# Kernel optimization log

Measured on AMD Instinct MI355X. Metric: run time of the kernel, lower is better.

The kernel has to match this reference:

```python
import jax, jax.numpy as jnp
import numpy as np

IH, IW, HEADS, DIM_HEAD = 32, 32, 8, 48
N = IH * IW
SCALE = DIM_HEAD ** -0.5
EPS = 1e-5


def _relative_index():
    # static precompute of relative distance indices, shape [N, N] int32
    yy, xx = np.meshgrid(np.arange(IH), np.arange(IW), indexing='ij')
    coords = np.stack([yy.ravel(), xx.ravel()])  # [2, N]
    rel = coords[:, :, None] - coords[:, None, :]  # [2, N, N]
    dist = np.ceil(np.sqrt(rel[0] ** 2 + rel[1] ** 2)).astype(np.int32)
    return jnp.asarray(dist)

REL_INDEX = _relative_index()


def _layernorm(x, w, b):
    mu = jnp.mean(x, axis=-1, keepdims=True)
    var = jnp.var(x, axis=-1, keepdims=True)
    return (x - mu) * jax.lax.rsqrt(var + EPS) * w + b


def setup_inputs() -> dict:
    key = jax.random.key(0)
    ks = jax.random.split(key, 8)
    d, inner, hid = 384, HEADS * DIM_HEAD, 1536
    return {
        'x': jax.random.normal(ks[0], (16, IH, IW, d), jnp.float32),
        'ln1_w': jnp.ones((d,), jnp.float32),
        'ln1_b': jnp.zeros((d,), jnp.float32),
        'w_qkv': jax.random.normal(ks[1], (d, 3 * inner), jnp.float32) * (d ** -0.5),
        'bias_table': jax.random.normal(ks[2], (45, HEADS), jnp.float32) * 0.02,
        'w_out': jax.random.normal(ks[3], (inner, d), jnp.float32) * (inner ** -0.5),
        'b_out': jnp.zeros((d,), jnp.float32),
        'ln2_w': jnp.ones((d,), jnp.float32),
        'ln2_b': jnp.zeros((d,), jnp.float32),
        'w1': jax.random.normal(ks[4], (d, hid), jnp.float32) * (d ** -0.5),
        'b1': jnp.zeros((hid,), jnp.float32),
        'w2': jax.random.normal(ks[5], (hid, d), jnp.float32) * (hid ** -0.5),
        'b2': jnp.zeros((d,), jnp.float32),
    }


def reference(x, ln1_w, ln1_b, w_qkv, bias_table, w_out, b_out,
              ln2_w, ln2_b, w1, b1, w2, b2):
    b = x.shape[0]
    xt = x.reshape(b, N, -1)  # b (ih iw) c

    # --- attention branch (PreNorm) ---
    h = _layernorm(xt, ln1_w, ln1_b)
    qkv = h @ w_qkv  # [b, N, 3*inner]
    q, k, v = jnp.split(qkv, 3, axis=-1)
    q = q.reshape(b, N, HEADS, DIM_HEAD).transpose(0, 2, 1, 3)
    k = k.reshape(b, N, HEADS, DIM_HEAD).transpose(0, 2, 1, 3)
    v = v.reshape(b, N, HEADS, DIM_HEAD).transpose(0, 2, 1, 3)
    dots = jnp.einsum('bhnd,bhmd->bhnm', q, k) * SCALE
    rel_bias = bias_table[REL_INDEX]  # [N, N, heads] gather
    dots = dots + rel_bias.transpose(2, 0, 1)[None]  # [1, h, N, N]
    attn = jax.nn.softmax(dots, axis=-1)
    out = jnp.einsum('bhnm,bhmd->bhnd', attn, v)
    out = out.transpose(0, 2, 1, 3).reshape(b, N, HEADS * DIM_HEAD)
    out = out @ w_out + b_out
    xt = xt + out

    # --- FFN branch (PreNorm) ---
    h = _layernorm(xt, ln2_w, ln2_b)
    h = jax.nn.gelu(h @ w1 + b1, approximate=False) @ w2 + b2
    xt = xt + h
    return xt.reshape(x.shape)
```

## Files before the change

### kernel.cpp

```cpp
#include <hip/hip_runtime.h>
#include <hip/hip_bf16.h>
#include <math.h>

typedef __bf16 bf16;
typedef __bf16 bf16x8 __attribute__((ext_vector_type(8)));
typedef __bf16 bf16x4 __attribute__((ext_vector_type(4)));
typedef float  f32x4  __attribute__((ext_vector_type(4)));

#define D_MODEL 384
#define HID     1536
#define NSEQ    1024
#define ROWS    16384
#define HEADS   8
#define DH      48
#define SCALE   0.14433756729740643f
#define MFIX    8.0f
#define BTAB_N  3969
#define BTAB_P  3972
#define KVT     4608
#define QP_BH   (NSEQ * DH)
#define KP_BH   (16 * KVT)

__device__ __forceinline__ void gload16(const void* g, void* l) {
    __builtin_amdgcn_global_load_lds((const __attribute__((address_space(1))) void*)g,
                                     (__attribute__((address_space(3))) void*)l, 16, 0, 0);
}

__device__ __forceinline__ float fast_gelu(float x) {
    float u = 0.7978845608f * fmaf(0.044715f * x * x, x, x);
    float e = __expf(2.f * u);
    float t = 1.f - 2.f * __builtin_amdgcn_rcpf(e + 1.f);
    return 0.5f * x * (1.f + t);
}

__global__ __launch_bounds__(256)
void bias_prep_kernel(const float* __restrict__ bias_table, float* __restrict__ Btab)
{
    int idx = blockIdx.x * 256 + threadIdx.x;
    if (idx >= BTAB_N) return;
    int dy = idx / 63 - 31, dx = idx % 63 - 31;
    int s2 = dy * dy + dx * dx;
    int r = (int)ceilf(sqrtf((float)s2));
    while (r * r < s2) ++r;
    while (r > 0 && (r - 1) * (r - 1) >= s2) --r;
#pragma unroll
    for (int h = 0; h < HEADS; ++h)
        Btab[h * BTAB_P + idx] = bias_table[r * HEADS + h] - MFIX;
}

__global__ __launch_bounds__(256)
void pack_init_kernel(bf16* __restrict__ Kp, bf16* __restrict__ Vp)
{
    const int bid = blockIdx.x, tid = threadIdx.x;
    if (bid < 512) {
        int row = bid * 256 + tid;
        bf16x8 z = {};
        bf16* p = Kp + (size_t)row * 72 + 48;
        *(bf16x8*)(p) = z;  *(bf16x8*)(p + 8) = z;  *(bf16x8*)(p + 16) = z;
    } else {
        int idx = (bid - 512) * 256 + tid;
        int tile = idx >> 4, rr = idx & 15;
        bf16 o = (bf16)1.f;
        bf16x8 ones = {o, o, o, o, o, o, o, o};
        bf16* p = Vp + (size_t)tile * KVT + (48 + rr) * 72;
#pragma unroll
        for (int c = 0; c < 9; ++c) *(bf16x8*)(p + c * 8) = ones;
    }
}

__global__ __launch_bounds__(256)
void wtrans_kernel(const float* __restrict__ in, bf16* __restrict__ out, int K, int N)
{
    __shared__ float T[64][65];
    const int k0 = blockIdx.y * 64, n0 = blockIdx.x * 64;
    const int rr = threadIdx.x >> 4, rc = threadIdx.x & 15;
#pragma unroll
    for (int i = 0; i < 4; ++i) {
        float4 v = *(const float4*)(in + (size_t)(k0 + rr + i * 16) * N + n0 + rc * 4);
        T[rr + i * 16][rc * 4 + 0] = v.x;  T[rr + i * 16][rc * 4 + 1] = v.y;
        T[rr + i * 16][rc * 4 + 2] = v.z;  T[rr + i * 16][rc * 4 + 3] = v.w;
    }
    __syncthreads();
#pragma unroll
    for (int i = 0; i < 4; ++i) {
        int n = rr + i * 16, kc = rc * 4;
        bf16x4 o;
        o[0] = (bf16)T[kc + 0][n];  o[1] = (bf16)T[kc + 1][n];
        o[2] = (bf16)T[kc + 2][n];  o[3] = (bf16)T[kc + 3][n];
        *(bf16x4*)(out + (size_t)(n0 + n) * K + k0 + kc) = o;
    }
}

__global__ __launch_bounds__(64)
void ln_kernel(const float* __restrict__ x, const float* __restrict__ w,
               const float* __restrict__ b, bf16* __restrict__ out)
{
    int row  = blockIdx.x;
    int lane = threadIdx.x;
    const float* xr = x + (size_t)row * D_MODEL;

    float v[6], s = 0.f, ss = 0.f;
#pragma unroll
    for (int i = 0; i < 6; ++i) {
        v[i] = xr[lane + i * 64];
        s  += v[i];
        ss += v[i] * v[i];
    }
#pragma unroll
    for (int off = 32; off; off >>= 1) {
        s  += __shfl_xor(s,  off);
        ss += __shfl_xor(ss, off);
    }
    float mu   = s * (1.f / D_MODEL);
    float var  = ss * (1.f / D_MODEL) - mu * mu;
    float rstd = rsqrtf(var + 1e-5f);

    bf16* orow = out + (size_t)row * D_MODEL;
#pragma unroll
    for (int i = 0; i < 6; ++i) {
        int c = lane + i * 64;
        orow[c] = (bf16)((v[i] - mu) * rstd * w[c] + b[c]);
    }
}

template<int EPI, typename CT>
__global__ __launch_bounds__(256)
void gemm3_kernel(const bf16* __restrict__ A, const bf16* __restrict__ BT,
                  CT* __restrict__ C, const float* __restrict__ bias,
                  const float* __restrict__ res, int nxblk, int Nn, int K,
                  bf16* __restrict__ qp, bf16* __restrict__ kp, bf16* __restrict__ vp)
{
    __shared__ alignas(16) bf16 As[128][64];
    __shared__ alignas(16) bf16 Bs[128][64];

    const int bid  = blockIdx.x;
    const int xcd  = bid & 7;
    const int slot = bid >> 3;
    const int yy   = slot / nxblk;
    const int m0   = (yy * 8 + xcd) * 128;
    const int n0   = (slot - yy * nxblk) * 128;

    const int tid  = threadIdx.x;
    const int w    = tid >> 6;
    const int lane = tid & 63;
    const int quad = lane >> 4;
    const int l16  = lane & 15;

    const int srow = lane >> 3;
    const int scol = (lane & 7) * 8;

    f32x4 acc[4][4] = {};

    for (int kt = 0; kt < K; kt += 64) {
        __syncthreads();
#pragma unroll
        for (int c = 0; c < 4; ++c) {
            const int ch = w * 4 + c;
            gload16(A  + (size_t)(m0 + ch * 8 + srow) * K + kt + scol, &As[ch * 8][0]);
            gload16(BT + (size_t)(n0 + ch * 8 + srow) * K + kt + scol, &Bs[ch * 8][0]);
        }
        __syncthreads();

#pragma unroll
        for (int kk = 0; kk < 2; ++kk) {
            bf16x8 af[4], bfr[4];
#pragma unroll
            for (int mt = 0; mt < 4; ++mt)
                af[mt] = *(const bf16x8*)(&As[(w & 1) * 64 + mt * 16 + l16][kk * 32 + quad * 8]);
#pragma unroll
            for (int nt = 0; nt < 4; ++nt)
                bfr[nt] = *(const bf16x8*)(&Bs[(w >> 1) * 64 + nt * 16 + l16][kk * 32 + quad * 8]);
#pragma unroll
            for (int mt = 0; mt < 4; ++mt)
#pragma unroll
                for (int nt = 0; nt < 4; ++nt)
                    acc[mt][nt] = __builtin_amdgcn_mfma_f32_16x16x32_bf16(
                        af[mt], bfr[nt], acc[mt][nt], 0, 0, 0);
        }
    }

#pragma unroll
    for (int mt = 0; mt < 4; ++mt) {
#pragma unroll
        for (int nt = 0; nt < 4; ++nt) {
            const int c0 = n0 + (w >> 1) * 64 + nt * 16;
            const int c  = c0 + l16;
            float bi = (EPI == 1 || EPI == 2) ? bias[c] : 0.f;
#pragma unroll
            for (int r = 0; r < 4; ++r) {
                int row = m0 + (w & 1) * 64 + mt * 16 + quad * 4 + r;
                float v = acc[mt][nt][r] + bi;
                if (EPI == 1) {
                    v += res[(size_t)row * Nn + c];
                    C[(size_t)row * Nn + c] = (CT)v;
                } else if (EPI == 2) {
                    v = fast_gelu(v);
                    C[(size_t)row * Nn + c] = (CT)v;
                } else {
                    int b   = row >> 10, seq = row & 1023;
                    if (c0 < 384) {
                        int h = c / 48, d = c - h * 48;
                        qp[(size_t)(b * 8 + h) * QP_BH + seq * 48 + d] = (bf16)(v * SCALE);
                    } else if (c0 < 768) {
                        int ck = c - 384;
                        int h = ck / 48, d = ck - h * 48;
                        kp[(size_t)(b * 8 + h) * KP_BH + (seq >> 6) * KVT
                           + (seq & 63) * 72 + d] = (bf16)v;
                    } else {
                        int cv = c - 768;
                        int h = cv / 48, d = cv - h * 48;
                        vp[(size_t)(b * 8 + h) * KP_BH + (seq >> 6) * KVT
                           + d * 72 + (seq & 63)] = (bf16)v;
                    }
                }
            }
        }
    }
}

__global__ __launch_bounds__(256)
void attn_kernel(const bf16* __restrict__ Qp, const bf16* __restrict__ Kp,
                 const bf16* __restrict__ Vp, const float* __restrict__ Btab,
                 bf16* __restrict__ out)
{
    __shared__ alignas(16) bf16 Ks[64][72];
    __shared__ alignas(16) bf16 Vs[64][72];
    __shared__ alignas(16) bf16 Ps[4][2][16][72];
    __shared__ alignas(16) float B2f[BTAB_P];

    const int bid  = blockIdx.x;
    const int xcd  = bid & 7;
    const int slot = bid >> 3;
    const int qc   = slot & 7;
    const int bh   = (slot >> 3) * 8 + xcd;
    const int q0   = qc * 128;
    const int tid  = threadIdx.x;
    const int wave = tid >> 6;
    const int lane = tid & 63;
    const int quad = lane >> 4;
    const int l16  = lane & 15;
    const int b    = bh >> 3, h = bh & 7;

    {
        const char* src = (const char*)(Btab + h * BTAB_P);
#pragma unroll
        for (int it = 0; it < 4; ++it) {
            int off = it * 4096 + tid * 16;
            if (off < BTAB_P * 4)
                gload16(src + off, (char*)B2f + it * 4096 + wave * 1024);
        }
    }

    bf16x8 qf0[2], qf1[2];
    int pi[2];
#pragma unroll
    for (int s = 0; s < 2; ++s) {
        int qrow = q0 + s * 64 + wave * 16 + l16;
        const bf16* qptr = Qp + (size_t)bh * QP_BH + qrow * 48;
        qf0[s] = *(const bf16x8*)(qptr + quad * 8);
#pragma unroll
        for (int c = 0; c < 8; ++c) qf1[s][c] = (bf16)0.f;
        if (quad < 2) qf1[s] = *(const bf16x8*)(qptr + 32 + quad * 8);
        pi[s] = (qrow >> 5) * 63 + (qrow & 31) + 31 * 63 + 31;
    }

    f32x4 o_acc[2][4] = {};

    for (int t = 0; t < 16; ++t) {
        const int n0 = t * 64;
        const bf16* kbase = Kp + (size_t)(bh * 16 + t) * KVT;
        const bf16* vbase = Vp + (size_t)(bh * 16 + t) * KVT;
        __syncthreads();
        for (int i = wave; i < 9; i += 4) {
            gload16(kbase + i * 512 + lane * 8, (bf16*)Ks + i * 512);
            gload16(vbase + i * 512 + lane * 8, (bf16*)Vs + i * 512);
        }
        __syncthreads();

        f32x4 sa[2][4] = {};
#pragma unroll
        for (int nt = 0; nt < 4; ++nt) {
            bf16x8 a0 = *(const bf16x8*)(&Ks[nt * 16 + l16][quad * 8]);
            bf16x8 a1 = *(const bf16x8*)(&Ks[nt * 16 + l16][32 + quad * 8]);
#pragma unroll
            for (int s = 0; s < 2; ++s) {
                sa[s][nt] = __builtin_amdgcn_mfma_f32_16x16x32_bf16(a0, qf0[s], sa[s][nt], 0, 0, 0);
                sa[s][nt] = __builtin_amdgcn_mfma_f32_16x16x32_bf16(a1, qf1[s], sa[s][nt], 0, 0, 0);
            }
        }

#pragma unroll
        for (int s = 0; s < 2; ++s)
#pragma unroll
            for (int nt = 0; nt < 4; ++nt) {
                const int j0 = n0 + nt * 16 + quad * 4;
                const int ib = pi[s] - ((j0 >> 5) * 63 + (j0 & 31));
                bf16x4 pk;
#pragma unroll
                for (int r = 0; r < 4; ++r)
                    pk[r] = (bf16)__expf(sa[s][nt][r] + B2f[ib - r]);
                *(bf16x4*)(&Ps[wave][s][l16][nt * 16 + quad * 4]) = pk;
            }

#pragma unroll
        for (int kk = 0; kk < 2; ++kk) {
            bf16x8 vf[4];
#pragma unroll
            for (int d = 0; d < 4; ++d)
                vf[d] = *(const bf16x8*)(&Vs[d * 16 + l16][kk * 32 + quad * 8]);
#pragma unroll
            for (int s = 0; s < 2; ++s) {
                bf16x8 pf = *(const bf16x8*)(&Ps[wave][s][l16][kk * 32 + quad * 8]);
#pragma unroll
                for (int d = 0; d < 4; ++d)
                    o_acc[s][d] = __builtin_amdgcn_mfma_f32_16x16x32_bf16(
                        pf, vf[d], o_acc[s][d], 0, 0, 0);
            }
        }
    }

#pragma unroll
    for (int s = 0; s < 2; ++s)
#pragma unroll
        for (int r = 0; r < 4; ++r) {
            float inv = 1.f / o_acc[s][3][r];
            int row = q0 + s * 64 + wave * 16 + quad * 4 + r;
            bf16* orow = out + ((size_t)b * NSEQ + row) * D_MODEL + h * DH;
#pragma unroll
            for (int d = 0; d < 3; ++d)
                orow[d * 16 + l16] = (bf16)(o_acc[s][d][r] * inv);
        }
}

extern "C" void kernel_launch(void* const* d_in, const int* in_sizes, int n_in,
                              void* d_out, int out_size, void* d_ws, size_t ws_size,
                              hipStream_t stream)
{
    const float* x          = (const float*)d_in[0];
    const float* ln1_w      = (const float*)d_in[1];
    const float* ln1_b      = (const float*)d_in[2];
    const float* w_qkv      = (const float*)d_in[3];
    const float* bias_table = (const float*)d_in[4];
    const float* w_out      = (const float*)d_in[5];
    const float* b_out      = (const float*)d_in[6];
    const float* ln2_w      = (const float*)d_in[7];
    const float* ln2_b      = (const float*)d_in[8];
    const float* w1         = (const float*)d_in[9];
    const float* b1         = (const float*)d_in[10];
    const float* w2         = (const float*)d_in[11];
    const float* b2         = (const float*)d_in[12];
    float* out = (float*)d_out;

    bf16* regA  = (bf16*)d_ws;
    bf16* Qpack = regA;
    bf16* Kpack = regA + 6291456;
    bf16* Vpack = regA + 15728640;
    bf16* regB  = regA + (size_t)ROWS * HID;
    bf16* wqkvT = regB + (size_t)ROWS * D_MODEL;
    bf16* woutT = wqkvT + 1152 * 384;
    bf16* w1T   = woutT + 384 * 384;
    bf16* w2T   = w1T + 1536 * 384;
    float* Btab = (float*)(w2T + 384 * 1536);
    float* x1   = out;

    bias_prep_kernel<<<(BTAB_N + 255) / 256, 256, 0, stream>>>(bias_table, Btab);
    pack_init_kernel<<<640, 256, 0, stream>>>(Kpack, Vpack);
    wtrans_kernel<<<dim3(1152 / 64, 384 / 64), 256, 0, stream>>>(w_qkv, wqkvT, 384, 1152);
    wtrans_kernel<<<dim3(384 / 64, 384 / 64), 256, 0, stream>>>(w_out, woutT, 384, 384);
    wtrans_kernel<<<dim3(1536 / 64, 384 / 64), 256, 0, stream>>>(w1, w1T, 384, 1536);
    wtrans_kernel<<<dim3(384 / 64, 1536 / 64), 256, 0, stream>>>(w2, w2T, 1536, 384);

    ln_kernel<<<ROWS, 64, 0, stream>>>(x, ln1_w, ln1_b, regB);
    gemm3_kernel<3, bf16><<<(1152 / 128) * (ROWS / 128), 256, 0, stream>>>(
        regB, wqkvT, (bf16*)nullptr, nullptr, nullptr, 1152 / 128, 1152, D_MODEL,
        Qpack, Kpack, Vpack);
    attn_kernel<<<1024, 256, 0, stream>>>(Qpack, Kpack, Vpack, Btab, regB);
    gemm3_kernel<1, float><<<(D_MODEL / 128) * (ROWS / 128), 256, 0, stream>>>(
        regB, woutT, x1, b_out, x, D_MODEL / 128, D_MODEL, D_MODEL,
        nullptr, nullptr, nullptr);
    ln_kernel<<<ROWS, 64, 0, stream>>>(x1, ln2_w, ln2_b, regB);
    gemm3_kernel<2, bf16><<<(HID / 128) * (ROWS / 128), 256, 0, stream>>>(
        regB, w1T, regA, b1, nullptr, HID / 128, HID, D_MODEL,
        nullptr, nullptr, nullptr);
    gemm3_kernel<1, float><<<(D_MODEL / 128) * (ROWS / 128), 256, 0, stream>>>(
        regA, w2T, out, b2, x1, D_MODEL / 128, D_MODEL, HID,
        nullptr, nullptr, nullptr);
}
```

Baseline: 329.9 us.

## Shrink attention LDS with bf16 bias table, exp2 softmax, and wave priority

Stores the relative-position bias table as bf16 pre-scaled by log2(e) and folds log2(e) into the Q scale. The softmax then uses a native exp2 instead of expf, and the constant shift moves into the score accumulator initialisation. The P staging buffer is halved by processing the two query sub-tiles one after another, and MFMA sections are wrapped in s_setprio. Launch bounds now request 4 blocks per CU. Together these cut LDS use and per-element ALU work to raise occupancy, at some cost in bias precision.

```diff
diff --git a/kernel.cpp b/kernel.cpp
--- a/kernel.cpp
+++ b/kernel.cpp
@@ -14,9 +14,11 @@
 #define HEADS   8
 #define DH      48
 #define SCALE   0.14433756729740643f
-#define MFIX    8.0f
+#define LOG2E   1.4426950408889634f
+#define QSCALE  (SCALE * LOG2E)
+#define M0      (-8.0f * LOG2E)
 #define BTAB_N  3969
-#define BTAB_P  3972
+#define BTAB_P  4096
 #define KVT     4608
 #define QP_BH   (NSEQ * DH)
 #define KP_BH   (16 * KVT)
@@ -34,7 +36,7 @@
 }
 
 __global__ __launch_bounds__(256)
-void bias_prep_kernel(const float* __restrict__ bias_table, float* __restrict__ Btab)
+void bias_prep_kernel(const float* __restrict__ bias_table, bf16* __restrict__ Btab)
 {
     int idx = blockIdx.x * 256 + threadIdx.x;
     if (idx >= BTAB_N) return;
@@ -45,7 +47,7 @@
     while (r > 0 && (r - 1) * (r - 1) >= s2) --r;
 #pragma unroll
     for (int h = 0; h < HEADS; ++h)
-        Btab[h * BTAB_P + idx] = bias_table[r * HEADS + h] - MFIX;
+        Btab[h * BTAB_P + idx] = (bf16)(bias_table[r * HEADS + h] * LOG2E);
 }
 
 __global__ __launch_bounds__(256)
@@ -200,7 +202,7 @@
                     int b   = row >> 10, seq = row & 1023;
                     if (c0 < 384) {
                         int h = c / 48, d = c - h * 48;
-                        qp[(size_t)(b * 8 + h) * QP_BH + seq * 48 + d] = (bf16)(v * SCALE);
+                        qp[(size_t)(b * 8 + h) * QP_BH + seq * 48 + d] = (bf16)(v * QSCALE);
                     } else if (c0 < 768) {
                         int ck = c - 384;
                         int h = ck / 48, d = ck - h * 48;
@@ -218,15 +220,15 @@
     }
 }
 
-__global__ __launch_bounds__(256)
+__global__ __launch_bounds__(256, 4)
 void attn_kernel(const bf16* __restrict__ Qp, const bf16* __restrict__ Kp,
-                 const bf16* __restrict__ Vp, const float* __restrict__ Btab,
+                 const bf16* __restrict__ Vp, const bf16* __restrict__ Btab,
                  bf16* __restrict__ out)
 {
     __shared__ alignas(16) bf16 Ks[64][72];
     __shared__ alignas(16) bf16 Vs[64][72];
-    __shared__ alignas(16) bf16 Ps[4][2][16][72];
-    __shared__ alignas(16) float B2f[BTAB_P];
+    __shared__ alignas(16) bf16 Ps[4][16][72];
+    __shared__ alignas(16) bf16 B2h[BTAB_P];
 
     const int bid  = blockIdx.x;
     const int xcd  = bid & 7;
@@ -242,13 +244,9 @@
     const int b    = bh >> 3, h = bh & 7;
 
     {
-        const char* src = (const char*)(Btab + h * BTAB_P);
-#pragma unroll
-        for (int it = 0; it < 4; ++it) {
-            int off = it * 4096 + tid * 16;
-            if (off < BTAB_P * 4)
-                gload16(src + off, (char*)B2f + it * 4096 + wave * 1024);
-        }
+        const char* src = (const char*)(Btab + (size_t)h * BTAB_P);
+        gload16(src + tid * 16,        (char*)B2h + wave * 1024);
+        gload16(src + 4096 + tid * 16, (char*)B2h + 4096 + wave * 1024);
     }
 
     bf16x8 qf0[2], qf1[2];
@@ -277,7 +275,14 @@
         }
         __syncthreads();
 
-        f32x4 sa[2][4] = {};
+        f32x4 sa[2][4];
+#pragma unroll
+        for (int s = 0; s < 2; ++s)
+#pragma unroll
+            for (int nt = 0; nt < 4; ++nt)
+                sa[s][nt] = (f32x4){M0, M0, M0, M0};
+
+        __builtin_amdgcn_s_setprio(1);
 #pragma unroll
         for (int nt = 0; nt < 4; ++nt) {
             bf16x8 a0 = *(const bf16x8*)(&Ks[nt * 16 + l16][quad * 8]);
@@ -288,9 +293,10 @@
                 sa[s][nt] = __builtin_amdgcn_mfma_f32_16x16x32_bf16(a1, qf1[s], sa[s][nt], 0, 0, 0);
             }
         }
-
-#pragma unroll
-        for (int s = 0; s < 2; ++s)
+        __builtin_amdgcn_s_setprio(0);
+
+#pragma unroll
+        for (int s = 0; s < 2; ++s) {
 #pragma unroll
             for (int nt = 0; nt < 4; ++nt) {
                 const int j0 = n0 + nt * 16 + quad * 4;
@@ -298,24 +304,24 @@
                 bf16x4 pk;
 #pragma unroll
                 for (int r = 0; r < 4; ++r)
-                    pk[r] = (bf16)__expf(sa[s][nt][r] + B2f[ib - r]);
-                *(bf16x4*)(&Ps[wave][s][l16][nt * 16 + quad * 4]) = pk;
+                    pk[r] = (bf16)__builtin_amdgcn_exp2f(sa[s][nt][r] + (float)B2h[ib - r]);
+                *(bf16x4*)(&Ps[wave][l16][nt * 16 + quad * 4]) = pk;
             }
 
-#pragma unroll
-        for (int kk = 0; kk < 2; ++kk) {
-            bf16x8 vf[4];
-#pragma unroll
-            for (int d = 0; d < 4; ++d)
-                vf[d] = *(const bf16x8*)(&Vs[d * 16 + l16][kk * 32 + quad * 8]);
-#pragma unroll
-            for (int s = 0; s < 2; ++s) {
-                bf16x8 pf = *(const bf16x8*)(&Ps[wave][s][l16][kk * 32 + quad * 8]);
+            __builtin_amdgcn_s_setprio(1);
+#pragma unroll
+            for (int kk = 0; kk < 2; ++kk) {
+                bf16x8 vf[4];
+#pragma unroll
+                for (int d = 0; d < 4; ++d)
+                    vf[d] = *(const bf16x8*)(&Vs[d * 16 + l16][kk * 32 + quad * 8]);
+                bf16x8 pf = *(const bf16x8*)(&Ps[wave][l16][kk * 32 + quad * 8]);
 #pragma unroll
                 for (int d = 0; d < 4; ++d)
                     o_acc[s][d] = __builtin_amdgcn_mfma_f32_16x16x32_bf16(
                         pf, vf[d], o_acc[s][d], 0, 0, 0);
             }
+            __builtin_amdgcn_s_setprio(0);
         }
     }
 
@@ -360,7 +366,7 @@
     bf16* woutT = wqkvT + 1152 * 384;
     bf16* w1T   = woutT + 384 * 384;
     bf16* w2T   = w1T + 1536 * 384;
-    float* Btab = (float*)(w2T + 384 * 1536);
+    bf16* Btab  = w2T + 384 * 1536;
     float* x1   = out;
 
     bias_prep_kernel<<<(BTAB_N + 255) / 256, 256, 0, stream>>>(bias_table, Btab);
```

Result: slower. 365.8 us (+10.9%).
